# Kernel tuning notes

Measured on AMD Instinct MI355X. Metric: run time of the kernel, lower is better.

Reference implementation:

```python
import jax, jax.numpy as jnp
import numpy as np

N, C, D, V, NC = 60000, 4, 200, 5000, 250


def _lin(key, out_d, in_d):
    # torch nn.Linear default init: U(-1/sqrt(in), 1/sqrt(in))
    s = 1.0 / np.sqrt(in_d)
    k1, k2 = jax.random.split(key)
    w = jax.random.uniform(k1, (out_d, in_d), minval=-s, maxval=s, dtype=jnp.float32)
    b = jax.random.uniform(k2, (out_d,), minval=-s, maxval=s, dtype=jnp.float32)
    return w, b


def setup_inputs() -> dict:
    key = jax.random.key(0)
    ks = jax.random.split(key, 16)
    inp = {}
    inp['tokens'] = jax.random.randint(ks[0], (N,), 0, V)
    inp['child_c'] = jax.random.normal(ks[1], (N, C, D), dtype=jnp.float32)
    inp['child_h'] = jax.random.normal(ks[2], (N, C, D), dtype=jnp.float32)
    inp['emb'] = jax.random.normal(ks[3], (V, D), dtype=jnp.float32)
    # ForBlock: proj1: 3D->D, proj2: 2D->D
    inp['p1_w'], inp['p1_b'] = _lin(ks[4], D, 3 * D)
    inp['p2_w'], inp['p2_b'] = _lin(ks[5], D, 2 * D)
    # treelstm gates (each Linear D->D)
    for i, g in enumerate(['ix', 'ih', 'fx', 'fh', 'ux', 'uh', 'ox', 'oh']):
        w, b = _lin(ks[6 + i], D, D)
        inp[g + '_w'], inp[g + '_b'] = w, b
    inp['fc2_w'], inp['fc2_b'] = _lin(ks[14], NC, D)
    return inp


def reference(tokens, child_c, child_h, emb,
              p1_w, p1_b, p2_w, p2_b,
              ix_w, ix_b, ih_w, ih_b, fx_w, fx_b, fh_w, fh_b,
              ux_w, ux_b, uh_w, uh_b, ox_w, ox_b, oh_w, oh_b,
              fc2_w, fc2_b):
    x = emb[tokens]  # [N, D] node token embeddings (nn.Embedding lookup)
    # ForBlock: control = relu(proj1(cat[init, cond, next])); hsum = relu(proj2(cat[control, block]))
    control = jax.nn.relu(
        jnp.concatenate([child_h[:, 0], child_h[:, 1], child_h[:, 2]], axis=-1) @ p1_w.T + p1_b)
    child_h_sum = jax.nn.relu(
        jnp.concatenate([control, child_h[:, 3]], axis=-1) @ p2_w.T + p2_b)  # [N, D]
    # treelstm.node update (vectorized over N nodes, C children)
    i = jax.nn.sigmoid(x @ ix_w.T + ix_b + child_h_sum @ ih_w.T + ih_b)
    o = jax.nn.sigmoid(x @ ox_w.T + ox_b + child_h_sum @ oh_w.T + oh_b)
    u = jnp.tanh(x @ ux_w.T + ux_b + child_h_sum @ uh_w.T + uh_b)
    fx = (x @ fx_w.T + fx_b)[:, None, :]  # [N, 1, D]
    f = jax.nn.sigmoid(jnp.einsum('ncd,md->ncm', child_h, fh_w) + fh_b + fx)  # [N, C, D]
    c = i * u + jnp.sum(f * child_c, axis=1)  # [N, D]
    h = o * jnp.tanh(c)  # [N, D]
    logits = h @ fc2_w.T + fc2_b  # [N, n_class]
    return logits
```

## Files before the change

### kernel.cpp

```cpp
#include <hip/hip_runtime.h>
#include <cmath>

#define NNODES 60000
#define DDIM   200
#define NCLS   250

constexpr int R   = 64;
constexpr int BK  = 32;
constexpr int XP  = 232;

typedef float  f32x4  __attribute__((ext_vector_type(4)));
typedef short  short8 __attribute__((ext_vector_type(8)));

constexpr int W_P1  = 0;
constexpr int W_P2A = 155648;
constexpr int W_P2B = 212992;
constexpr int W_FX  = 270336;
constexpr int W_FH  = 327680;
constexpr int W_IX  = 385024;
constexpr int W_IH  = 442368;
constexpr int W_UX  = 499712;
constexpr int W_UH  = 557056;
constexpr int W_OX  = 614400;
constexpr int W_OH  = 671744;
constexpr int W_FC2 = 729088;
constexpr int W_TOTAL_ELEMS = 786432;
constexpr size_t W_TOTAL_BYTES = (size_t)W_TOTAL_ELEMS * 2;

__device__ __forceinline__ short f2b(float f) {
    union { float f; unsigned u; } x; x.f = f;
    unsigned r = (x.u + 0x7FFFu + ((x.u >> 16) & 1u)) >> 16;
    return (short)r;
}
__device__ __forceinline__ float b2f(short s) {
    union { unsigned u; float f; } x; x.u = ((unsigned)(unsigned short)s) << 16;
    return x.f;
}
__device__ __forceinline__ float sgm(float x)  { return 1.0f / (1.0f + __expf(-x)); }
__device__ __forceinline__ float tanh_fast(float x) { return 1.0f - 2.0f / (__expf(2.0f * x) + 1.0f); }
__device__ __forceinline__ int   swz(int b)    { return b ^ (((b >> 7) & 3) << 4); }

__global__ void wprep(const float* __restrict__ p1w, const float* __restrict__ p2w,
                      const float* __restrict__ fxw, const float* __restrict__ fhw,
                      const float* __restrict__ ixw, const float* __restrict__ ihw,
                      const float* __restrict__ uxw, const float* __restrict__ uhw,
                      const float* __restrict__ oxw, const float* __restrict__ ohw,
                      const float* __restrict__ fc2w, short* __restrict__ ws)
{
    int i = blockIdx.x * 256 + threadIdx.x;
    if (i >= W_TOTAL_ELEMS) return;
    float v = 0.0f;
    if (i < W_P2A) {
        int n = i / 608, k = i % 608;
        if (n < 200 && k < 600) v = p1w[n * 600 + k];
        ws[i] = f2b(v); return;
    }
    int j = i - W_P2A;
    int m = j / 57344, rem = j % 57344;
    int n = rem / 224, k = rem % 224;
    const float* src; int stride = 200, off = 0, ncols = 200;
    switch (m) {
        case 0:  src = p2w; stride = 400; break;
        case 1:  src = p2w; stride = 400; off = 200; break;
        case 2:  src = fxw; break;
        case 3:  src = fhw; break;
        case 4:  src = ixw; break;
        case 5:  src = ihw; break;
        case 6:  src = uxw; break;
        case 7:  src = uhw; break;
        case 8:  src = oxw; break;
        case 9:  src = ohw; break;
        default: src = fc2w; ncols = 250; break;
    }
    if (n < ncols && k < 200) v = src[n * stride + off + k];
    ws[i] = f2b(v);
}

__device__ __forceinline__ void gload16(const void* g, void* l) {
    __builtin_amdgcn_global_load_lds((const __attribute__((address_space(1))) unsigned*)g,
                                     (__attribute__((address_space(3))) unsigned*)l, 16, 0, 0);
}

__device__ __forceinline__ void stage_w(const short* __restrict__ wmat, int Kpad, int t,
                                        int wrows, int wv, short* w_sw)
{
    const int issues = wrows >> 4;
    for (int q = wv; q < issues; q += 4) {
        const int lane = threadIdx.x & 63;
        const int db = q * 1024 + lane * 16;
        const int n  = db >> 6;
        const int g  = (db >> 4) & 3;
        const int gs = g ^ ((n >> 1) & 3);
        const short* src = wmat + (long)n * Kpad + t * BK + gs * 8;
        char* dst = ((char*)w_sw) + q * 1024;
        gload16(src, dst);
    }
}

__device__ __forceinline__ void stage_a_chh(short* a_sw, const float* __restrict__ ag,
                                            int row0, int colofs, int k0, int Kreal, int tid)
{
    const int r = tid >> 2, gq = tid & 3;
    long rg = row0 + r; if (rg >= NNODES) rg = NNODES - 1;
    const float* src = ag + rg * 800 + colofs + k0 + gq * 8;
    short8 v;
    if (k0 + BK <= Kreal) {
        float4 f0 = *(const float4*)(src);
        float4 f1 = *(const float4*)(src + 4);
        v[0] = f2b(f0.x); v[1] = f2b(f0.y); v[2] = f2b(f0.z); v[3] = f2b(f0.w);
        v[4] = f2b(f1.x); v[5] = f2b(f1.y); v[6] = f2b(f1.z); v[7] = f2b(f1.w);
    } else {
        #pragma unroll
        for (int i = 0; i < 8; ++i) {
            int k = k0 + gq * 8 + i;
            float f = (k < Kreal) ? src[i] : 0.0f;
            v[i] = f2b(f);
        }
    }
    int b = r * 64 + gq * 16; b = swz(b);
    *(short8*)((char*)a_sw + b) = v;
}

template<int NF, bool FROM_GLOBAL>
__device__ __forceinline__ void gemm_pass(
    f32x4 (*acc)[8],
    const short (*Ap)[XP],
    const float* __restrict__ ag, int row0, int colofs, int Kreal,
    const short* __restrict__ wmat, int ktiles, int Kpad, int wrows,
    short* a_sw, short* w_sw,
    int tid, int wv, int wm, int wn, int l15, int lg)
{
    for (int t = 0; t < ktiles; ++t) {
        __syncthreads();
        stage_w(wmat, Kpad, t, wrows, wv, w_sw);
        if constexpr (FROM_GLOBAL)
            stage_a_chh(a_sw, ag, row0, colofs, t * BK, Kreal, tid);
        __syncthreads();
        short8 af[2];
        #pragma unroll
        for (int mi = 0; mi < 2; ++mi) {
            const int row = wm * 32 + mi * 16 + l15;
            if constexpr (FROM_GLOBAL) {
                int b = swz(row * 64 + lg * 16);
                af[mi] = *(const short8*)((const char*)a_sw + b);
            } else {
                af[mi] = *(const short8*)&Ap[row][t * BK + lg * 8];
            }
        }
        #pragma unroll
        for (int ni = 0; ni < NF; ++ni) {
            const int n = (wn * NF + ni) * 16 + l15;
            int b = swz(n * 64 + lg * 16);
            short8 bf = *(const short8*)((const char*)w_sw + b);
            #pragma unroll
            for (int mi = 0; mi < 2; ++mi)
                acc[mi][ni] = __builtin_amdgcn_mfma_f32_16x16x32_bf16(af[mi], bf, acc[mi][ni], 0, 0, 0);
        }
    }
}

#define ZERO_ACC()  { _Pragma("unroll") for (int mi_=0; mi_<2; ++mi_) { _Pragma("unroll") for (int ni_=0; ni_<8; ++ni_) { _Pragma("unroll") for (int q_=0;q_<4;++q_) acc[mi_][ni_][q_] = 0.0f; } } }

__global__ __launch_bounds__(256, 2)
void fused_mfma(const int* __restrict__ tok,
                const float* __restrict__ chc,
                const float* __restrict__ chh,
                const float* __restrict__ emb,
                const float* __restrict__ p1b_, const float* __restrict__ p2b_,
                const float* __restrict__ ixb, const float* __restrict__ ihb,
                const float* __restrict__ fxb, const float* __restrict__ fhb,
                const float* __restrict__ uxb, const float* __restrict__ uhb,
                const float* __restrict__ oxb, const float* __restrict__ ohb,
                const float* __restrict__ fc2b,
                const short* __restrict__ ws,
                float* __restrict__ out)
{
    __shared__ __align__(16) short x_lds[R][XP];
    __shared__ __align__(16) short hbuf[R][XP];
    __shared__ __align__(16) short a_sw[R * BK];
    __shared__ __align__(16) short w_sw[8192];

    const int tid = threadIdx.x;
    const int wv = tid >> 6, wm = wv >> 1, wn = wv & 1;
    const int l15 = tid & 15, lg = (tid & 63) >> 4;
    const int row0 = blockIdx.x * R;

    {
        const int r = tid >> 2, q = tid & 3;
        #pragma unroll
        for (int c = 200 + q * 8; c < 200 + q * 8 + 8; ++c) { x_lds[r][c] = 0; hbuf[r][c] = 0; }
        long rg = row0 + r; if (rg >= NNODES) rg = NNODES - 1;
        const float* er = emb + (long)tok[rg] * DDIM;
        const int c0 = q * 50;
        #pragma unroll
        for (int i = 0; i < 50; i += 2) {
            float2 f = *(const float2*)(er + c0 + i);
            x_lds[r][c0 + i]     = f2b(f.x);
            x_lds[r][c0 + i + 1] = f2b(f.y);
        }
    }

    f32x4 acc[2][8];

    ZERO_ACC();
    gemm_pass<7, true>(acc, nullptr, chh, row0, 0, 600, ws + W_P1, 19, 608, 224,
                       a_sw, w_sw, tid, wv, wm, wn, l15, lg);
    #pragma unroll
    for (int mi = 0; mi < 2; ++mi)
        #pragma unroll
        for (int ni = 0; ni < 7; ++ni) {
            const int col = (wn * 7 + ni) * 16 + l15;
            if (col < DDIM) {
                const float b = p1b_[col];
                #pragma unroll
                for (int j = 0; j < 4; ++j) {
                    const int lrow = wm * 32 + mi * 16 + lg * 4 + j;
                    hbuf[lrow][col] = f2b(fmaxf(acc[mi][ni][j] + b, 0.0f));
                }
            }
        }

    ZERO_ACC();
    gemm_pass<7, false>(acc, hbuf, nullptr, 0, 0, 0, ws + W_P2A, 7, 224, 224,
                        a_sw, w_sw, tid, wv, wm, wn, l15, lg);
    gemm_pass<7, true>(acc, nullptr, chh, row0, 600, 200, ws + W_P2B, 7, 224, 224,
                       a_sw, w_sw, tid, wv, wm, wn, l15, lg);
    #pragma unroll
    for (int mi = 0; mi < 2; ++mi)
        #pragma unroll
        for (int ni = 0; ni < 7; ++ni) {
            const int col = (wn * 7 + ni) * 16 + l15;
            if (col < DDIM) {
                const float b = p2b_[col];
                #pragma unroll
                for (int j = 0; j < 4; ++j) {
                    const int lrow = wm * 32 + mi * 16 + lg * 4 + j;
                    hbuf[lrow][col] = f2b(fmaxf(acc[mi][ni][j] + b, 0.0f));
                }
            }
        }

    float giu[2][7][4];
    ZERO_ACC();
    gemm_pass<7, false>(acc, x_lds, nullptr, 0, 0, 0, ws + W_IX, 7, 224, 224,
                        a_sw, w_sw, tid, wv, wm, wn, l15, lg);
    gemm_pass<7, false>(acc, hbuf, nullptr, 0, 0, 0, ws + W_IH, 7, 224, 224,
                        a_sw, w_sw, tid, wv, wm, wn, l15, lg);
    #pragma unroll
    for (int mi = 0; mi < 2; ++mi)
        #pragma unroll
        for (int ni = 0; ni < 7; ++ni) {
            const int col = (wn * 7 + ni) * 16 + l15;
            const float b = (col < DDIM) ? (ixb[col] + ihb[col]) : 0.0f;
            #pragma unroll
            for (int j = 0; j < 4; ++j) giu[mi][ni][j] = sgm(acc[mi][ni][j] + b);
        }

    ZERO_ACC();
    gemm_pass<7, false>(acc, x_lds, nullptr, 0, 0, 0, ws + W_UX, 7, 224, 224,
                        a_sw, w_sw, tid, wv, wm, wn, l15, lg);
    gemm_pass<7, false>(acc, hbuf, nullptr, 0, 0, 0, ws + W_UH, 7, 224, 224,
                        a_sw, w_sw, tid, wv, wm, wn, l15, lg);
    #pragma unroll
    for (int mi = 0; mi < 2; ++mi)
        #pragma unroll
        for (int ni = 0; ni < 7; ++ni) {
            const int col = (wn * 7 + ni) * 16 + l15;
            const float b = (col < DDIM) ? (uxb[col] + uhb[col]) : 0.0f;
            #pragma unroll
            for (int j = 0; j < 4; ++j) giu[mi][ni][j] *= tanh_fast(acc[mi][ni][j] + b);
        }

    ZERO_ACC();
    gemm_pass<7, false>(acc, x_lds, nullptr, 0, 0, 0, ws + W_OX, 7, 224, 224,
                        a_sw, w_sw, tid, wv, wm, wn, l15, lg);
    gemm_pass<7, false>(acc, hbuf, nullptr, 0, 0, 0, ws + W_OH, 7, 224, 224,
                        a_sw, w_sw, tid, wv, wm, wn, l15, lg);
    __syncthreads();
    #pragma unroll
    for (int mi = 0; mi < 2; ++mi)
        #pragma unroll
        for (int ni = 0; ni < 7; ++ni) {
            const int col = (wn * 7 + ni) * 16 + l15;
            if (col < DDIM) {
                const float b = oxb[col] + ohb[col];
                #pragma unroll
                for (int j = 0; j < 4; ++j) {
                    const int lrow = wm * 32 + mi * 16 + lg * 4 + j;
                    hbuf[lrow][col] = f2b(sgm(acc[mi][ni][j] + b));
                }
            }
        }

    float fxr[2][7][4];
    ZERO_ACC();
    gemm_pass<7, false>(acc, x_lds, nullptr, 0, 0, 0, ws + W_FX, 7, 224, 224,
                        a_sw, w_sw, tid, wv, wm, wn, l15, lg);
    #pragma unroll
    for (int mi = 0; mi < 2; ++mi)
        #pragma unroll
        for (int ni = 0; ni < 7; ++ni) {
            const int col = (wn * 7 + ni) * 16 + l15;
            const float b = (col < DDIM) ? fxb[col] : 0.0f;
            #pragma unroll
            for (int j = 0; j < 4; ++j) fxr[mi][ni][j] = acc[mi][ni][j] + b;
        }

    __syncthreads();
    #pragma unroll
    for (int mi = 0; mi < 2; ++mi)
        #pragma unroll
        for (int ni = 0; ni < 7; ++ni) {
            const int col = (wn * 7 + ni) * 16 + l15;
            if (col < DDIM) {
                #pragma unroll
                for (int j = 0; j < 4; ++j) {
                    const int lrow = wm * 32 + mi * 16 + lg * 4 + j;
                    x_lds[lrow][col] = f2b(giu[mi][ni][j]);
                }
            }
        }

    float csum[2][7][4];
    #pragma unroll
    for (int mi = 0; mi < 2; ++mi)
        #pragma unroll
        for (int ni = 0; ni < 7; ++ni)
            #pragma unroll
            for (int j = 0; j < 4; ++j) csum[mi][ni][j] = 0.0f;

    for (int c = 0; c < 4; ++c) {
        ZERO_ACC();
        gemm_pass<7, true>(acc, nullptr, chh, row0, c * 200, 200, ws + W_FH, 7, 224, 224,
                           a_sw, w_sw, tid, wv, wm, wn, l15, lg);
        #pragma unroll
        for (int mi = 0; mi < 2; ++mi)
            #pragma unroll
            for (int ni = 0; ni < 7; ++ni) {
                const int col = (wn * 7 + ni) * 16 + l15;
                if (col < DDIM) {
                    const float b = fhb[col];
                    #pragma unroll
                    for (int j = 0; j < 4; ++j) {
                        const int lrow = wm * 32 + mi * 16 + lg * 4 + j;
                        long rg = row0 + lrow; if (rg >= NNODES) rg = NNODES - 1;
                        const float cv = chc[rg * 800 + c * 200 + col];
                        csum[mi][ni][j] += sgm(acc[mi][ni][j] + b + fxr[mi][ni][j]) * cv;
                    }
                }
            }
    }

    #pragma unroll
    for (int mi = 0; mi < 2; ++mi)
        #pragma unroll
        for (int ni = 0; ni < 7; ++ni) {
            const int col = (wn * 7 + ni) * 16 + l15;
            if (col < DDIM) {
                #pragma unroll
                for (int j = 0; j < 4; ++j) {
                    const int lrow = wm * 32 + mi * 16 + lg * 4 + j;
                    const float iu = b2f(x_lds[lrow][col]);
                    const float o  = b2f(hbuf[lrow][col]);
                    const float cc = iu + csum[mi][ni][j];
                    hbuf[lrow][col] = f2b(o * tanh_fast(cc));
                }
            }
        }

    ZERO_ACC();
    gemm_pass<8, false>(acc, hbuf, nullptr, 0, 0, 0, ws + W_FC2, 7, 224, 256,
                        a_sw, w_sw, tid, wv, wm, wn, l15, lg);
    #pragma unroll
    for (int mi = 0; mi < 2; ++mi)
        #pragma unroll
        for (int ni = 0; ni < 8; ++ni) {
            const int col = (wn * 8 + ni) * 16 + l15;
            if (col < NCLS) {
                const float b = fc2b[col];
                #pragma unroll
                for (int j = 0; j < 4; ++j) {
                    const int lrow = wm * 32 + mi * 16 + lg * 4 + j;
                    const long gr = row0 + lrow;
                    if (gr < NNODES) out[gr * NCLS + col] = acc[mi][ni][j] + b;
                }
            }
        }
}

constexpr int FRT = 32, FBK = 16, FNT = 256, FRTP = FRT + 4, FBUFP = 208;
__device__ __forceinline__ float sgm_f(float x) { return 1.0f / (1.0f + expf(-x)); }

__device__ __forceinline__ void f_stage(
    float (*aT)[FRTP], float (*wt)[FNT], int row0, int k0,
    const float* a1g, int a1pitch, const int* gidx, const float* a1l, int a1lp, int K1,
    const float* a2g, int a2pitch, const float* a2l, int a2lp, int K2,
    const float* wa, int wap, int KW1, const float* wb, int wbp,
    int ncols, int tid)
{
    const int Ktot = K1 + K2;
    {
        const int kk = tid & 15, k = k0 + kk;
        #pragma unroll
        for (int h = 0; h < 2; ++h) {
            const int r = (tid >> 4) + h * 16;
            float v = 0.0f;
            if (k < K1) {
                if (a1l) v = a1l[r * a1lp + k];
                else {
                    const long rb = gidx ? (long)gidx[row0 + r] * a1pitch : (long)(row0 + r) * a1pitch;
                    v = a1g[rb + k];
                }
            } else if (k < Ktot) {
                if (a2l) v = a2l[r * a2lp + (k - K1)];
                else     v = a2g[(long)(row0 + r) * a2pitch + (k - K1)];
            }
            aT[kk][r] = v;
        }
    }
    {
        const int col = tid;
        #pragma unroll
        for (int kk = 0; kk < FBK; ++kk) {
            const int k = k0 + kk; float v = 0.0f;
            if (col < ncols && k < Ktot) {
                if (k < KW1) v = wa[(long)col * wap + k];
                else         v = wb[(long)col * wbp + (k - KW1)];
            }
            wt[kk][col] = v;
        }
    }
}
__device__ __forceinline__ void f_gemm(
    float (*aT)[FRTP], float (*wt)[FNT], float acc[8][4], int row0,
    const float* a1g, int a1p, const int* gidx, const float* a1l, int a1lp, int K1,
    const float* a2g, int a2p, const float* a2l, int a2lp, int K2,
    const float* wa, int wap, int KW1, const float* wb, int wbp,
    int ncols, int tid, int tr, int tc)
{
    #pragma unroll
    for (int j = 0; j < 8; ++j)
        #pragma unroll
        for (int i = 0; i < 4; ++i) acc[j][i] = 0.0f;
    const int Ktot = K1 + K2;
    for (int k0 = 0; k0 < Ktot; k0 += FBK) {
        __syncthreads();
        f_stage(aT, wt, row0, k0, a1g, a1p, gidx, a1l, a1lp, K1, a2g, a2p, a2l, a2lp, K2,
                wa, wap, KW1, wb, wbp, ncols, tid);
        __syncthreads();
        #pragma unroll
        for (int kk = 0; kk < FBK; ++kk) {
            const float w0 = wt[kk][tc*4+0], w1 = wt[kk][tc*4+1], w2 = wt[kk][tc*4+2], w3 = wt[kk][tc*4+3];
            #pragma unroll
            for (int j = 0; j < 8; ++j) {
                const float a = aT[kk][tr*8+j];
                acc[j][0] = fmaf(a, w0, acc[j][0]); acc[j][1] = fmaf(a, w1, acc[j][1]);
                acc[j][2] = fmaf(a, w2, acc[j][2]); acc[j][3] = fmaf(a, w3, acc[j][3]);
            }
        }
    }
}
__global__ __launch_bounds__(256)
void fused_fp32(const int* tok, const float* chc, const float* chh, const float* emb,
                const float* p1w, const float* p1b, const float* p2w, const float* p2b,
                const float* ixw, const float* ixb, const float* ihw, const float* ihb,
                const float* fxw, const float* fxb, const float* fhw, const float* fhb,
                const float* uxw, const float* uxb, const float* uhw, const float* uhb,
                const float* oxw, const float* oxb, const float* ohw, const float* ohb,
                const float* fc2w, const float* fc2b, float* out)
{
    __shared__ float aT[FBK][FRTP]; __shared__ float wt[FBK][FNT]; __shared__ float buf[FRT][FBUFP];
    const int tid = threadIdx.x, tr = tid >> 6, tc = tid & 63, c0 = tc * 4;
    const int row0 = blockIdx.x * FRT;
    float acc[8][4];
    f_gemm(aT, wt, acc, row0, chh, 800, nullptr, nullptr, 0, 600, nullptr,0,nullptr,0,0, p1w,600,600,nullptr,0, DDIM, tid,tr,tc);
    if (c0 < DDIM) { const float4 b = *(const float4*)&p1b[c0];
        #pragma unroll
        for (int j=0;j<8;++j){int r=tr*8+j; buf[r][c0]=fmaxf(acc[j][0]+b.x,0.f); buf[r][c0+1]=fmaxf(acc[j][1]+b.y,0.f); buf[r][c0+2]=fmaxf(acc[j][2]+b.z,0.f); buf[r][c0+3]=fmaxf(acc[j][3]+b.w,0.f);} }
    f_gemm(aT, wt, acc, row0, nullptr,0,nullptr,&buf[0][0],FBUFP,200, chh+600,800,nullptr,0,200, p2w,400,400,nullptr,0, DDIM, tid,tr,tc);
    if (c0 < DDIM) { const float4 b = *(const float4*)&p2b[c0];
        #pragma unroll
        for (int j=0;j<8;++j){int r=tr*8+j; buf[r][c0]=fmaxf(acc[j][0]+b.x,0.f); buf[r][c0+1]=fmaxf(acc[j][1]+b.y,0.f); buf[r][c0+2]=fmaxf(acc[j][2]+b.z,0.f); buf[r][c0+3]=fmaxf(acc[j][3]+b.w,0.f);} }
    f_gemm(aT, wt, acc, row0, emb, DDIM, tok, nullptr,0,200, nullptr,0,nullptr,0,0, fxw,200,200,nullptr,0, DDIM, tid,tr,tc);
    float fxr[8][4];
    { float4 b = make_float4(0,0,0,0); if (c0<DDIM) b = *(const float4*)&fxb[c0];
      #pragma unroll
      for (int j=0;j<8;++j){fxr[j][0]=acc[j][0]+b.x;fxr[j][1]=acc[j][1]+b.y;fxr[j][2]=acc[j][2]+b.z;fxr[j][3]=acc[j][3]+b.w;} }
    float csum[8][4];
    #pragma unroll
    for (int j=0;j<8;++j)
        #pragma unroll
        for (int i=0;i<4;++i) csum[j][i]=0.f;
    for (int cc_=0; cc_<4; ++cc_) {
        f_gemm(aT, wt, acc, row0, chh+cc_*200,800,nullptr,nullptr,0,200, nullptr,0,nullptr,0,0, fhw,200,200,nullptr,0, DDIM, tid,tr,tc);
        if (c0 < DDIM) { const float4 b = *(const float4*)&fhb[c0];
            #pragma unroll
            for (int j=0;j<8;++j){ const long r=row0+tr*8+j; const float4 cv=*(const float4*)&chc[r*800+cc_*200+c0];
                csum[j][0]+=sgm_f(acc[j][0]+b.x+fxr[j][0])*cv.x; csum[j][1]+=sgm_f(acc[j][1]+b.y+fxr[j][1])*cv.y;
                csum[j][2]+=sgm_f(acc[j][2]+b.z+fxr[j][2])*cv.z; csum[j][3]+=sgm_f(acc[j][3]+b.w+fxr[j][3])*cv.w; } }
    }
    f_gemm(aT, wt, acc, row0, emb, DDIM, tok, nullptr,0,200, nullptr,0,&buf[0][0],FBUFP,200, ixw,200,200,ihw,200, DDIM, tid,tr,tc);
    float gi[8][4];
    { float4 b1=make_float4(0,0,0,0),b2=b1; if(c0<DDIM){b1=*(const float4*)&ixb[c0];b2=*(const float4*)&ihb[c0];}
      #pragma unroll
      for(int j=0;j<8;++j){gi[j][0]=sgm_f(acc[j][0]+b1.x+b2.x);gi[j][1]=sgm_f(acc[j][1]+b1.y+b2.y);gi[j][2]=sgm_f(acc[j][2]+b1.z+b2.z);gi[j][3]=sgm_f(acc[j][3]+b1.w+b2.w);} }
    f_gemm(aT, wt, acc, row0, emb, DDIM, tok, nullptr,0,200, nullptr,0,&buf[0][0],FBUFP,200, uxw,200,200,uhw,200, DDIM, tid,tr,tc);
    float cval[8][4];
    { float4 b1=make_float4(0,0,0,0),b2=b1; if(c0<DDIM){b1=*(const float4*)&uxb[c0];b2=*(const float4*)&uhb[c0];}
      #pragma unroll
      for(int j=0;j<8;++j){cval[j][0]=gi[j][0]*tanhf(acc[j][0]+b1.x+b2.x)+csum[j][0];cval[j][1]=gi[j][1]*tanhf(acc[j][1]+b1.y+b2.y)+csum[j][1];
                           cval[j][2]=gi[j][2]*tanhf(acc[j][2]+b1.z+b2.z)+csum[j][2];cval[j][3]=gi[j][3]*tanhf(acc[j][3]+b1.w+b2.w)+csum[j][3];} }
    f_gemm(aT, wt, acc, row0, emb, DDIM, tok, nullptr,0,200, nullptr,0,&buf[0][0],FBUFP,200, oxw,200,200,ohw,200, DDIM, tid,tr,tc);
    if (c0 < DDIM) { const float4 b1=*(const float4*)&oxb[c0], b2=*(const float4*)&ohb[c0];
        #pragma unroll
        for(int j=0;j<8;++j){int r=tr*8+j;
            buf[r][c0]=sgm_f(acc[j][0]+b1.x+b2.x)*tanhf(cval[j][0]); buf[r][c0+1]=sgm_f(acc[j][1]+b1.y+b2.y)*tanhf(cval[j][1]);
            buf[r][c0+2]=sgm_f(acc[j][2]+b1.z+b2.z)*tanhf(cval[j][2]); buf[r][c0+3]=sgm_f(acc[j][3]+b1.w+b2.w)*tanhf(cval[j][3]);} }
    f_gemm(aT, wt, acc, row0, nullptr,0,nullptr,&buf[0][0],FBUFP,200, nullptr,0,nullptr,0,0, fc2w,200,200,nullptr,0, NCLS, tid,tr,tc);
    #pragma unroll
    for (int j=0;j<8;++j){ const long r=row0+tr*8+j;
        #pragma unroll
        for (int i=0;i<4;++i){ const int col=c0+i; if (col<NCLS) out[r*NCLS+col]=acc[j][i]+fc2b[col]; } }
}

extern "C" void kernel_launch(void* const* d_in, const int* in_sizes, int n_in,
                              void* d_out, int out_size, void* d_ws, size_t ws_size,
                              hipStream_t stream)
{
    const int*   tok  = (const int*)  d_in[0];
    const float* chc  = (const float*)d_in[1];
    const float* chh  = (const float*)d_in[2];
    const float* emb  = (const float*)d_in[3];
    const float* p1w  = (const float*)d_in[4];
    const float* p1b  = (const float*)d_in[5];
    const float* p2w  = (const float*)d_in[6];
    const float* p2b  = (const float*)d_in[7];
    const float* ixw  = (const float*)d_in[8];
    const float* ixb  = (const float*)d_in[9];
    const float* ihw  = (const float*)d_in[10];
    const float* ihb  = (const float*)d_in[11];
    const float* fxw  = (const float*)d_in[12];
    const float* fxb  = (const float*)d_in[13];
    const float* fhw  = (const float*)d_in[14];
    const float* fhb  = (const float*)d_in[15];
    const float* uxw  = (const float*)d_in[16];
    const float* uxb  = (const float*)d_in[17];
    const float* uhw  = (const float*)d_in[18];
    const float* uhb  = (const float*)d_in[19];
    const float* oxw  = (const float*)d_in[20];
    const float* oxb  = (const float*)d_in[21];
    const float* ohw  = (const float*)d_in[22];
    const float* ohb  = (const float*)d_in[23];
    const float* fc2w = (const float*)d_in[24];
    const float* fc2b = (const float*)d_in[25];
    float* out = (float*)d_out;

    if (ws_size >= W_TOTAL_BYTES) {
        short* ws = (short*)d_ws;
        hipLaunchKernelGGL(wprep, dim3((W_TOTAL_ELEMS + 255) / 256), dim3(256), 0, stream,
                           p1w, p2w, fxw, fhw, ixw, ihw, uxw, uhw, oxw, ohw, fc2w, ws);
        hipLaunchKernelGGL(fused_mfma, dim3((NNODES + R - 1) / R), dim3(256), 0, stream,
                           tok, chc, chh, emb,
                           p1b, p2b, ixb, ihb, fxb, fhb, uxb, uhb, oxb, ohb, fc2b,
                           ws, out);
    } else {
        hipLaunchKernelGGL(fused_fp32, dim3(NNODES / FRT), dim3(256), 0, stream,
                           tok, chc, chh, emb, p1w, p1b, p2w, p2b,
                           ixw, ixb, ihw, ihb, fxw, fxb, fhw, fhb,
                           uxw, uxb, uhw, uhb, oxw, oxb, ohw, ohb, fc2w, fc2b, out);
    }
}
```

Baseline: 363.8 us.

## Rewrite fused MFMA kernel with 32-row tiles, double-buffered staging, packed bf16 converts

```diff
diff --git a/kernel.cpp b/kernel.cpp
--- a/kernel.cpp
+++ b/kernel.cpp
@@ -5,9 +5,17 @@
 #define DDIM   200
 #define NCLS   250
 
-constexpr int R   = 64;
+constexpr int R   = 32;
 constexpr int BK  = 32;
-constexpr int XP  = 232;
+constexpr int XP  = 208;
+
+constexpr int O_X  = 0;
+constexpr int O_H  = R * XP;
+constexpr int O_A  = 2 * R * XP;
+constexpr int AS   = R * BK;
+constexpr int O_W  = O_A + 2 * AS;
+constexpr int WS   = 8192;
+constexpr int SH_TOT = O_W + 2 * WS + 32;
 
 typedef float  f32x4  __attribute__((ext_vector_type(4)));
 typedef short  short8 __attribute__((ext_vector_type(8)));
@@ -32,13 +40,26 @@
     unsigned r = (x.u + 0x7FFFu + ((x.u >> 16) & 1u)) >> 16;
     return (short)r;
 }
+__device__ __forceinline__ unsigned cvtpk(float lo, float hi) {
+    unsigned r; asm("v_cvt_pk_bf16_f32 %0, %1, %2" : "=v"(r) : "v"(lo), "v"(hi));
+    return r;
+}
+__device__ __forceinline__ short f2b1(float f) { return (short)(cvtpk(f, f) & 0xffffu); }
 __device__ __forceinline__ float b2f(short s) {
     union { unsigned u; float f; } x; x.u = ((unsigned)(unsigned short)s) << 16;
     return x.f;
 }
+__device__ __forceinline__ float b2f_lo(unsigned u) { return b2f((short)(u & 0xffffu)); }
+__device__ __forceinline__ float b2f_hi(unsigned u) { return b2f((short)(u >> 16)); }
 __device__ __forceinline__ float sgm(float x)  { return 1.0f / (1.0f + __expf(-x)); }
 __device__ __forceinline__ float tanh_fast(float x) { return 1.0f - 2.0f / (__expf(2.0f * x) + 1.0f); }
 __device__ __forceinline__ int   swz(int b)    { return b ^ (((b >> 7) & 3) << 4); }
+__device__ __forceinline__ short8 cvt8(float4 f0, float4 f1) {
+    union { unsigned u[4]; short8 s; } c;
+    c.u[0] = cvtpk(f0.x, f0.y); c.u[1] = cvtpk(f0.z, f0.w);
+    c.u[2] = cvtpk(f1.x, f1.y); c.u[3] = cvtpk(f1.z, f1.w);
+    return c.s;
+}
 
 __global__ void wprep(const float* __restrict__ p1w, const float* __restrict__ p2w,
                       const float* __restrict__ fxw, const float* __restrict__ fhw,
@@ -100,15 +121,14 @@
 __device__ __forceinline__ void stage_a_chh(short* a_sw, const float* __restrict__ ag,
                                             int row0, int colofs, int k0, int Kreal, int tid)
 {
+    if (tid >= 4 * R) return;
     const int r = tid >> 2, gq = tid & 3;
-    long rg = row0 + r; if (rg >= NNODES) rg = NNODES - 1;
-    const float* src = ag + rg * 800 + colofs + k0 + gq * 8;
+    const float* src = ag + (long)(row0 + r) * 800 + colofs + k0 + gq * 8;
     short8 v;
     if (k0 + BK <= Kreal) {
         float4 f0 = *(const float4*)(src);
         float4 f1 = *(const float4*)(src + 4);
-        v[0] = f2b(f0.x); v[1] = f2b(f0.y); v[2] = f2b(f0.z); v[3] = f2b(f0.w);
-        v[4] = f2b(f1.x); v[5] = f2b(f1.y); v[6] = f2b(f1.z); v[7] = f2b(f1.w);
+        v = cvt8(f0, f1);
     } else {
         #pragma unroll
         for (int i = 0; i < 8; ++i) {
@@ -123,62 +143,64 @@
 
 template<int NF, bool FROM_GLOBAL>
 __device__ __forceinline__ void gemm_pass(
-    f32x4 (*acc)[8],
-    const short (*Ap)[XP],
+    f32x4 (&acc)[NF],
+    const short* __restrict__ Ap,
     const float* __restrict__ ag, int row0, int colofs, int Kreal,
     const short* __restrict__ wmat, int ktiles, int Kpad, int wrows,
     short* a_sw, short* w_sw,
     int tid, int wv, int wm, int wn, int l15, int lg)
 {
+    stage_w(wmat, Kpad, 0, wrows, wv, w_sw);
+    if constexpr (FROM_GLOBAL)
+        stage_a_chh(a_sw, ag, row0, colofs, 0, Kreal, tid);
+    asm volatile("s_waitcnt vmcnt(0) lgkmcnt(0)" ::: "memory");
+    __builtin_amdgcn_s_barrier();
     for (int t = 0; t < ktiles; ++t) {
-        __syncthreads();
-        stage_w(wmat, Kpad, t, wrows, wv, w_sw);
+        const int cur = t & 1, nxt = cur ^ 1;
+        if (t + 1 < ktiles) {
+            stage_w(wmat, Kpad, t + 1, wrows, wv, w_sw + nxt * WS);
+            if constexpr (FROM_GLOBAL)
+                stage_a_chh(a_sw + nxt * AS, ag, row0, colofs, (t + 1) * BK, Kreal, tid);
+        }
+        short8 af;
+        const int row = wm * 16 + l15;
         if constexpr (FROM_GLOBAL)
-            stage_a_chh(a_sw, ag, row0, colofs, t * BK, Kreal, tid);
-        __syncthreads();
-        short8 af[2];
-        #pragma unroll
-        for (int mi = 0; mi < 2; ++mi) {
-            const int row = wm * 32 + mi * 16 + l15;
-            if constexpr (FROM_GLOBAL) {
-                int b = swz(row * 64 + lg * 16);
-                af[mi] = *(const short8*)((const char*)a_sw + b);
-            } else {
-                af[mi] = *(const short8*)&Ap[row][t * BK + lg * 8];
-            }
-        }
+            af = *(const short8*)((const char*)(a_sw + cur * AS) + swz(row * 64 + lg * 16));
+        else
+            af = *(const short8*)(Ap + row * XP + t * BK + lg * 8);
         #pragma unroll
         for (int ni = 0; ni < NF; ++ni) {
             const int n = (wn * NF + ni) * 16 + l15;
-            int b = swz(n * 64 + lg * 16);
-            short8 bf = *(const short8*)((const char*)w_sw + b);
-            #pragma unroll
-            for (int mi = 0; mi < 2; ++mi)
-                acc[mi][ni] = __builtin_amdgcn_mfma_f32_16x16x32_bf16(af[mi], bf, acc[mi][ni], 0, 0, 0);
-        }
-    }
-}
-
-#define ZERO_ACC()  { _Pragma("unroll") for (int mi_=0; mi_<2; ++mi_) { _Pragma("unroll") for (int ni_=0; ni_<8; ++ni_) { _Pragma("unroll") for (int q_=0;q_<4;++q_) acc[mi_][ni_][q_] = 0.0f; } } }
+            short8 bf = *(const short8*)((const char*)(w_sw + cur * WS) + swz(n * 64 + lg * 16));
+            acc[ni] = __builtin_amdgcn_mfma_f32_16x16x32_bf16(af, bf, acc[ni], 0, 0, 0);
+        }
+        asm volatile("s_waitcnt vmcnt(0) lgkmcnt(0)" ::: "memory");
+        __builtin_amdgcn_s_barrier();
+    }
+}
+
+#define Z7(A)  { _Pragma("unroll") for (int z_=0; z_<7; ++z_) { _Pragma("unroll") for (int q_=0;q_<4;++q_) A[z_][q_] = 0.0f; } }
+#define Z8(A)  { _Pragma("unroll") for (int z_=0; z_<8; ++z_) { _Pragma("unroll") for (int q_=0;q_<4;++q_) A[z_][q_] = 0.0f; } }
 
 __global__ __launch_bounds__(256, 2)
-void fused_mfma(const int* __restrict__ tok,
-                const float* __restrict__ chc,
-                const float* __restrict__ chh,
-                const float* __restrict__ emb,
-                const float* __restrict__ p1b_, const float* __restrict__ p2b_,
-                const float* __restrict__ ixb, const float* __restrict__ ihb,
-                const float* __restrict__ fxb, const float* __restrict__ fhb,
-                const float* __restrict__ uxb, const float* __restrict__ uhb,
-                const float* __restrict__ oxb, const float* __restrict__ ohb,
-                const float* __restrict__ fc2b,
-                const short* __restrict__ ws,
-                float* __restrict__ out)
-{
-    __shared__ __align__(16) short x_lds[R][XP];
-    __shared__ __align__(16) short hbuf[R][XP];
-    __shared__ __align__(16) short a_sw[R * BK];
-    __shared__ __align__(16) short w_sw[8192];
+void fused_v7(const int* __restrict__ tok,
+              const float* __restrict__ chc,
+              const float* __restrict__ chh,
+              const float* __restrict__ emb,
+              const float* __restrict__ p1b_, const float* __restrict__ p2b_,
+              const float* __restrict__ ixb, const float* __restrict__ ihb,
+              const float* __restrict__ fxb, const float* __restrict__ fhb,
+              const float* __restrict__ uxb, const float* __restrict__ uhb,
+              const float* __restrict__ oxb, const float* __restrict__ ohb,
+              const float* __restrict__ fc2b,
+              const short* __restrict__ ws,
+              float* __restrict__ out)
+{
+    __shared__ __align__(16) short SH[SH_TOT];
+    short* X    = SH + O_X;
+    short* H    = SH + O_H;
+    short* a_sw = SH + O_A;
+    short* w_sw = SH + O_W;
 
     const int tid = threadIdx.x;
     const int wv = tid >> 6, wm = wv >> 1, wn = wv & 1;
@@ -186,206 +208,170 @@
     const int row0 = blockIdx.x * R;
 
     {
-        const int r = tid >> 2, q = tid & 3;
-        #pragma unroll
-        for (int c = 200 + q * 8; c < 200 + q * 8 + 8; ++c) { x_lds[r][c] = 0; hbuf[r][c] = 0; }
-        long rg = row0 + r; if (rg >= NNODES) rg = NNODES - 1;
-        const float* er = emb + (long)tok[rg] * DDIM;
-        const int c0 = q * 50;
-        #pragma unroll
-        for (int i = 0; i < 50; i += 2) {
-            float2 f = *(const float2*)(er + c0 + i);
-            x_lds[r][c0 + i]     = f2b(f.x);
-            x_lds[r][c0 + i + 1] = f2b(f.y);
-        }
-    }
-
-    f32x4 acc[2][8];
-
-    ZERO_ACC();
-    gemm_pass<7, true>(acc, nullptr, chh, row0, 0, 600, ws + W_P1, 19, 608, 224,
-                       a_sw, w_sw, tid, wv, wm, wn, l15, lg);
-    #pragma unroll
-    for (int mi = 0; mi < 2; ++mi)
+        short8 z = (short8)0;
+        short8* shv = (short8*)SH;
+        #pragma unroll 1
+        for (int i = tid; i < SH_TOT / 8; i += 256) shv[i] = z;
+    }
+    __syncthreads();
+    {
+        #pragma unroll
+        for (int it = 0; it < 4; ++it) {
+            int u = tid + it * 256;
+            if (u < 800) {
+                int r = u / 25, cu = (u % 25) * 8;
+                const float* s = emb + (long)tok[row0 + r] * DDIM + cu;
+                float4 f0 = *(const float4*)s, f1 = *(const float4*)(s + 4);
+                *(short8*)(X + r * XP + cu) = cvt8(f0, f1);
+            }
+        }
+    }
+    __syncthreads();
+
+    f32x4 g[7];
+
+    unsigned fxr[7][2];
+    Z7(g);
+    gemm_pass<7, false>(g, X, nullptr, 0, 0, 0, ws + W_FX, 7, 224, 224,
+                        a_sw, w_sw, tid, wv, wm, wn, l15, lg);
+    #pragma unroll
+    for (int ni = 0; ni < 7; ++ni) {
+        const int col = (wn * 7 + ni) * 16 + l15;
+        const float b = (col < DDIM) ? fxb[col] : 0.0f;
+        fxr[ni][0] = cvtpk(g[ni][0] + b, g[ni][1] + b);
+        fxr[ni][1] = cvtpk(g[ni][2] + b, g[ni][3] + b);
+    }
+
+    float csum[7][4];
+    #pragma unroll
+    for (int ni = 0; ni < 7; ++ni)
+        #pragma unroll
+        for (int j = 0; j < 4; ++j) csum[ni][j] = 0.0f;
+
+    #pragma unroll 1
+    for (int c = 0; c < 4; ++c) {
+        Z7(g);
+        gemm_pass<7, true>(g, nullptr, chh, row0, c * 200, 200, ws + W_FH, 7, 224, 224,
+                           a_sw, w_sw, tid, wv, wm, wn, l15, lg);
         #pragma unroll
         for (int ni = 0; ni < 7; ++ni) {
             const int col = (wn * 7 + ni) * 16 + l15;
             if (col < DDIM) {
-                const float b = p1b_[col];
+                const float fb = fhb[col];
                 #pragma unroll
                 for (int j = 0; j < 4; ++j) {
-                    const int lrow = wm * 32 + mi * 16 + lg * 4 + j;
-                    hbuf[lrow][col] = f2b(fmaxf(acc[mi][ni][j] + b, 0.0f));
+                    const int lr = wm * 16 + lg * 4 + j;
+                    const float cv = chc[(long)(row0 + lr) * 800 + c * 200 + col];
+                    const unsigned pk = fxr[ni][j >> 1];
+                    const float fx = (j & 1) ? b2f_hi(pk) : b2f_lo(pk);
+                    csum[ni][j] += sgm(g[ni][j] + fb + fx) * cv;
                 }
             }
         }
-
-    ZERO_ACC();
-    gemm_pass<7, false>(acc, hbuf, nullptr, 0, 0, 0, ws + W_P2A, 7, 224, 224,
-                        a_sw, w_sw, tid, wv, wm, wn, l15, lg);
-    gemm_pass<7, true>(acc, nullptr, chh, row0, 600, 200, ws + W_P2B, 7, 224, 224,
+    }
+
+    Z7(g);
+    gemm_pass<7, true>(g, nullptr, chh, row0, 0, 600, ws + W_P1, 19, 608, 224,
                        a_sw, w_sw, tid, wv, wm, wn, l15, lg);
     #pragma unroll
-    for (int mi = 0; mi < 2; ++mi)
-        #pragma unroll
-        for (int ni = 0; ni < 7; ++ni) {
-            const int col = (wn * 7 + ni) * 16 + l15;
-            if (col < DDIM) {
-                const float b = p2b_[col];
-                #pragma unroll
-                for (int j = 0; j < 4; ++j) {
-                    const int lrow = wm * 32 + mi * 16 + lg * 4 + j;
-                    hbuf[lrow][col] = f2b(fmaxf(acc[mi][ni][j] + b, 0.0f));
-                }
-            }
-        }
-
-    float giu[2][7][4];
-    ZERO_ACC();
-    gemm_pass<7, false>(acc, x_lds, nullptr, 0, 0, 0, ws + W_IX, 7, 224, 224,
-                        a_sw, w_sw, tid, wv, wm, wn, l15, lg);
-    gemm_pass<7, false>(acc, hbuf, nullptr, 0, 0, 0, ws + W_IH, 7, 224, 224,
-                        a_sw, w_sw, tid, wv, wm, wn, l15, lg);
-    #pragma unroll
-    for (int mi = 0; mi < 2; ++mi)
-        #pragma unroll
-        for (int ni = 0; ni < 7; ++ni) {
-            const int col = (wn * 7 + ni) * 16 + l15;
-            const float b = (col < DDIM) ? (ixb[col] + ihb[col]) : 0.0f;
+    for (int ni = 0; ni < 7; ++ni) {
+        const int col = (wn * 7 + ni) * 16 + l15;
+        if (col < DDIM) {
+            const float b = p1b_[col];
             #pragma unroll
-            for (int j = 0; j < 4; ++j) giu[mi][ni][j] = sgm(acc[mi][ni][j] + b);
-        }
-
-    ZERO_ACC();
-    gemm_pass<7, false>(acc, x_lds, nullptr, 0, 0, 0, ws + W_UX, 7, 224, 224,
-                        a_sw, w_sw, tid, wv, wm, wn, l15, lg);
-    gemm_pass<7, false>(acc, hbuf, nullptr, 0, 0, 0, ws + W_UH, 7, 224, 224,
-                        a_sw, w_sw, tid, wv, wm, wn, l15, lg);
-    #pragma unroll
-    for (int mi = 0; mi < 2; ++mi)
-        #pragma unroll
-        for (int ni = 0; ni < 7; ++ni) {
-            const int col = (wn * 7 + ni) * 16 + l15;
-            const float b = (col < DDIM) ? (uxb[col] + uhb[col]) : 0.0f;
+            for (int j = 0; j < 4; ++j) {
+                const int lr = wm * 16 + lg * 4 + j;
+                H[lr * XP + col] = f2b1(fmaxf(g[ni][j] + b, 0.0f));
+            }
+        }
+    }
+    __syncthreads();
+
+    Z7(g);
+    gemm_pass<7, false>(g, H, nullptr, 0, 0, 0, ws + W_P2A, 7, 224, 224,
+                        a_sw, w_sw, tid, wv, wm, wn, l15, lg);
+    gemm_pass<7, true>(g, nullptr, chh, row0, 600, 200, ws + W_P2B, 7, 224, 224,
+                       a_sw, w_sw, tid, wv, wm, wn, l15, lg);
+    #pragma unroll
+    for (int ni = 0; ni < 7; ++ni) {
+        const int col = (wn * 7 + ni) * 16 + l15;
+        if (col < DDIM) {
+            const float b = p2b_[col];
             #pragma unroll
-            for (int j = 0; j < 4; ++j) giu[mi][ni][j] *= tanh_fast(acc[mi][ni][j] + b);
-        }
-
-    ZERO_ACC();
-    gemm_pass<7, false>(acc, x_lds, nullptr, 0, 0, 0, ws + W_OX, 7, 224, 224,
-                        a_sw, w_sw, tid, wv, wm, wn, l15, lg);
-    gemm_pass<7, false>(acc, hbuf, nullptr, 0, 0, 0, ws + W_OH, 7, 224, 224,
-                        a_sw, w_sw, tid, wv, wm, wn, l15, lg);
+            for (int j = 0; j < 4; ++j) {
+                const int lr = wm * 16 + lg * 4 + j;
+                H[lr * XP + col] = f2b1(fmaxf(g[ni][j] + b, 0.0f));
+            }
+        }
+    }
     __syncthreads();
-    #pragma unroll
-    for (int mi = 0; mi < 2; ++mi)
-        #pragma unroll
-        for (int ni = 0; ni < 7; ++ni) {
-            const int col = (wn * 7 + ni) * 16 + l15;
-            if (col < DDIM) {
-                const float b = oxb[col] + ohb[col];
-                #pragma unroll
-                for (int j = 0; j < 4; ++j) {
-                    const int lrow = wm * 32 + mi * 16 + lg * 4 + j;
-                    hbuf[lrow][col] = f2b(sgm(acc[mi][ni][j] + b));
-                }
-            }
-        }
-
-    float fxr[2][7][4];
-    ZERO_ACC();
-    gemm_pass<7, false>(acc, x_lds, nullptr, 0, 0, 0, ws + W_FX, 7, 224, 224,
-                        a_sw, w_sw, tid, wv, wm, wn, l15, lg);
-    #pragma unroll
-    for (int mi = 0; mi < 2; ++mi)
-        #pragma unroll
-        for (int ni = 0; ni < 7; ++ni) {
-            const int col = (wn * 7 + ni) * 16 + l15;
-            const float b = (col < DDIM) ? fxb[col] : 0.0f;
+
+    unsigned gi[7][2];
+    Z7(g);
+    gemm_pass<7, false>(g, X, nullptr, 0, 0, 0, ws + W_IX, 7, 224, 224,
+                        a_sw, w_sw, tid, wv, wm, wn, l15, lg);
+    gemm_pass<7, false>(g, H, nullptr, 0, 0, 0, ws + W_IH, 7, 224, 224,
+                        a_sw, w_sw, tid, wv, wm, wn, l15, lg);
+    #pragma unroll
+    for (int ni = 0; ni < 7; ++ni) {
+        const int col = (wn * 7 + ni) * 16 + l15;
+        const float b = (col < DDIM) ? (ixb[col] + ihb[col]) : 0.0f;
+        gi[ni][0] = cvtpk(sgm(g[ni][0] + b), sgm(g[ni][1] + b));
+        gi[ni][1] = cvtpk(sgm(g[ni][2] + b), sgm(g[ni][3] + b));
+    }
+
+    Z7(g);
+    gemm_pass<7, false>(g, X, nullptr, 0, 0, 0, ws + W_UX, 7, 224, 224,
+                        a_sw, w_sw, tid, wv, wm, wn, l15, lg);
+    gemm_pass<7, false>(g, H, nullptr, 0, 0, 0, ws + W_UH, 7, 224, 224,
+                        a_sw, w_sw, tid, wv, wm, wn, l15, lg);
+    #pragma unroll
+    for (int ni = 0; ni < 7; ++ni) {
+        const int col = (wn * 7 + ni) * 16 + l15;
+        const float b = (col < DDIM) ? (uxb[col] + uhb[col]) : 0.0f;
+        #pragma unroll
+        for (int j = 0; j < 4; ++j) {
+            const unsigned pk = gi[ni][j >> 1];
+            const float iv = (j & 1) ? b2f_hi(pk) : b2f_lo(pk);
+            csum[ni][j] = iv * tanh_fast(g[ni][j] + b) + csum[ni][j];
+        }
+    }
+
+    Z7(g);
+    gemm_pass<7, false>(g, X, nullptr, 0, 0, 0, ws + W_OX, 7, 224, 224,
+                        a_sw, w_sw, tid, wv, wm, wn, l15, lg);
+    gemm_pass<7, false>(g, H, nullptr, 0, 0, 0, ws + W_OH, 7, 224, 224,
+                        a_sw, w_sw, tid, wv, wm, wn, l15, lg);
+    #pragma unroll
+    for (int ni = 0; ni < 7; ++ni) {
+        const int col = (wn * 7 + ni) * 16 + l15;
+        if (col < DDIM) {
+            const float b = oxb[col] + ohb[col];
             #pragma unroll
-            for (int j = 0; j < 4; ++j) fxr[mi][ni][j] = acc[mi][ni][j] + b;
-        }
-
+            for (int j = 0; j < 4; ++j) {
+                const int lr = wm * 16 + lg * 4 + j;
+                H[lr * XP + col] = f2b1(sgm(g[ni][j] + b) * tanh_fast(csum[ni][j]));
+            }
+        }
+    }
     __syncthreads();
-    #pragma unroll
-    for (int mi = 0; mi < 2; ++mi)
-        #pragma unroll
-        for (int ni = 0; ni < 7; ++ni) {
-            const int col = (wn * 7 + ni) * 16 + l15;
-            if (col < DDIM) {
-                #pragma unroll
-                for (int j = 0; j < 4; ++j) {
-                    const int lrow = wm * 32 + mi * 16 + lg * 4 + j;
-                    x_lds[lrow][col] = f2b(giu[mi][ni][j]);
-                }
-            }
-        }
-
-    float csum[2][7][4];
-    #pragma unroll
-    for (int mi = 0; mi < 2; ++mi)
-        #pragma unroll
-        for (int ni = 0; ni < 7; ++ni)
+
+    f32x4 o8[8];
+    Z8(o8);
+    gemm_pass<8, false>(o8, H, nullptr, 0, 0, 0, ws + W_FC2, 7, 224, 256,
+                        a_sw, w_sw, tid, wv, wm, wn, l15, lg);
+    #pragma unroll
+    for (int ni = 0; ni < 8; ++ni) {
+        const int col = (wn * 8 + ni) * 16 + l15;
+        if (col < NCLS) {
+            const float b = fc2b[col];
             #pragma unroll
-            for (int j = 0; j < 4; ++j) csum[mi][ni][j] = 0.0f;
-
-    for (int c = 0; c < 4; ++c) {
-        ZERO_ACC();
-        gemm_pass<7, true>(acc, nullptr, chh, row0, c * 200, 200, ws + W_FH, 7, 224, 224,
-                           a_sw, w_sw, tid, wv, wm, wn, l15, lg);
-        #pragma unroll
-        for (int mi = 0; mi < 2; ++mi)
-            #pragma unroll
-            for (int ni = 0; ni < 7; ++ni) {
-                const int col = (wn * 7 + ni) * 16 + l15;
-                if (col < DDIM) {
-                    const float b = fhb[col];
-                    #pragma unroll
-                    for (int j = 0; j < 4; ++j) {
-                        const int lrow = wm * 32 + mi * 16 + lg * 4 + j;
-                        long rg = row0 + lrow; if (rg >= NNODES) rg = NNODES - 1;
-                        const float cv = chc[rg * 800 + c * 200 + col];
-                        csum[mi][ni][j] += sgm(acc[mi][ni][j] + b + fxr[mi][ni][j]) * cv;
-                    }
-                }
-            }
-    }
-
-    #pragma unroll
-    for (int mi = 0; mi < 2; ++mi)
-        #pragma unroll
-        for (int ni = 0; ni < 7; ++ni) {
-            const int col = (wn * 7 + ni) * 16 + l15;
-            if (col < DDIM) {
-                #pragma unroll
-                for (int j = 0; j < 4; ++j) {
-                    const int lrow = wm * 32 + mi * 16 + lg * 4 + j;
-                    const float iu = b2f(x_lds[lrow][col]);
-                    const float o  = b2f(hbuf[lrow][col]);
-                    const float cc = iu + csum[mi][ni][j];
-                    hbuf[lrow][col] = f2b(o * tanh_fast(cc));
-                }
-            }
-        }
-
-    ZERO_ACC();
-    gemm_pass<8, false>(acc, hbuf, nullptr, 0, 0, 0, ws + W_FC2, 7, 224, 256,
-                        a_sw, w_sw, tid, wv, wm, wn, l15, lg);
-    #pragma unroll
-    for (int mi = 0; mi < 2; ++mi)
-        #pragma unroll
-        for (int ni = 0; ni < 8; ++ni) {
-            const int col = (wn * 8 + ni) * 16 + l15;
-            if (col < NCLS) {
-                const float b = fc2b[col];
-                #pragma unroll
-                for (int j = 0; j < 4; ++j) {
-                    const int lrow = wm * 32 + mi * 16 + lg * 4 + j;
-                    const long gr = row0 + lrow;
-                    if (gr < NNODES) out[gr * NCLS + col] = acc[mi][ni][j] + b;
-                }
-            }
-        }
+            for (int j = 0; j < 4; ++j) {
+                const int lr = wm * 16 + lg * 4 + j;
+                out[(long)(row0 + lr) * NCLS + col] = o8[ni][j] + b;
+            }
+        }
+    }
 }
 
 constexpr int FRT = 32, FBK = 16, FNT = 256, FRTP = FRT + 4, FBUFP = 208;
@@ -559,7 +545,7 @@
         short* ws = (short*)d_ws;
         hipLaunchKernelGGL(wprep, dim3((W_TOTAL_ELEMS + 255) / 256), dim3(256), 0, stream,
                            p1w, p2w, fxw, fhw, ixw, ihw, uxw, uhw, oxw, ohw, fc2w, ws);
-        hipLaunchKernelGGL(fused_mfma, dim3((NNODES + R - 1) / R), dim3(256), 0, stream,
+        hipLaunchKernelGGL(fused_v7, dim3(NNODES / R), dim3(256), 0, stream,
                            tok, chc, chh, emb,
                            p1b, p2b, ixb, ihb, fxb, fhb, uxb, uhb, oxb, ohb, fc2b,
                            ws, out);
```

After: 449.8 us. 1.24x slower.
